# Kernel tuning notes

Hardware: AMD Instinct MI355X
Metric: run time of the kernel (lower is better)

## Reference

```python
import jax, jax.numpy as jnp
import numpy as np

DIM = 256

def setup_inputs() -> dict:
    key = jax.random.key(0)
    ks = jax.random.split(key, 7)
    s = 1.0 / np.sqrt(DIM)
    x = jax.random.normal(ks[0], (16, DIM, 32, 32), dtype=jnp.float32)
    proj_w = jax.random.uniform(ks[1], (DIM, DIM), jnp.float32, -s, s)
    proj_b = jax.random.uniform(ks[2], (DIM,), jnp.float32, -s, s)
    w1 = jax.random.uniform(ks[3], (DIM, DIM), jnp.float32, -s, s)
    b1 = jax.random.uniform(ks[4], (DIM,), jnp.float32, -s, s)
    w2 = jax.random.uniform(ks[5], (DIM, DIM), jnp.float32, -s, s)
    b2 = jax.random.uniform(ks[6], (DIM,), jnp.float32, -s, s)
    return {"x": x, "proj_w": proj_w, "proj_b": proj_b, "w1": w1, "b1": b1, "w2": w2, "b2": b2}

def reference(x, proj_w, proj_b, w1, b1, w2, b2):
    B, C, H, W = x.shape
    # nodes: [B, N, C] with N = H*W
    nodes = x.reshape(B, C, H * W).transpose(0, 2, 1)
    q = nodes @ proj_w.T + proj_b                      # [B,N,C]
    scores = jnp.einsum('bnc,bmc->bnm', q, q) / jnp.sqrt(jnp.float32(C))
    attn = jax.nn.softmax(scores, axis=-1)             # [B,N,N]
    agg = jnp.einsum('bnm,bmc->bnc', attn, nodes)      # [B,N,C]
    h = jax.nn.gelu(agg @ w1.T + b1, approximate=False)
    out = h @ w2.T + b2                                # [B,N,C]
    return x + out.transpose(0, 2, 1).reshape(B, C, H, W)
```

## Files before the change

kernel.cpp:

```cpp
#include <hip/hip_runtime.h>
#include <stdint.h>

typedef unsigned short u16;
typedef unsigned char u8;
typedef __attribute__((ext_vector_type(8))) short short8;
typedef __attribute__((ext_vector_type(4))) float f32x4;

#define NB    16
#define DIM   256
#define NTOK  1024

__device__ __forceinline__ u16 f2b(float f) {
    union { float f; uint32_t u; } v; v.f = f;
    uint32_t u = v.u;
    u += 0x7fffu + ((u >> 16) & 1u);
    return (u16)(u >> 16);
}
__device__ __forceinline__ uint32_t pack2(float a, float b) {
    return (uint32_t)f2b(a) | ((uint32_t)f2b(b) << 16);
}
__device__ __forceinline__ f32x4 mfma16(short8 a, short8 b, f32x4 c) {
    return __builtin_amdgcn_mfma_f32_16x16x32_bf16(a, b, c, 0, 0, 0);
}
__device__ __forceinline__ f32x4 mfma_fp8(long a, long b, f32x4 c) {
    return __builtin_amdgcn_mfma_f32_16x16x32_fp8_fp8(a, b, c, 0, 0, 0);
}
__device__ __forceinline__ short8 ld8(const u16* p) {
    return *reinterpret_cast<const short8*>(p);
}
__device__ __forceinline__ uint32_t pk4fp8(float a, float b, float c, float d) {
    uint32_t u = (uint32_t)__builtin_amdgcn_cvt_pk_fp8_f32(a, b, 0, false);
    u = (uint32_t)__builtin_amdgcn_cvt_pk_fp8_f32(c, d, (int)u, true);
    return u;
}
__device__ __forceinline__ u8 pk1fp8(float a) {
    return (u8)(__builtin_amdgcn_cvt_pk_fp8_f32(a, a, 0, false) & 0xff);
}
__device__ __forceinline__ void gl_lds(const void* g, void* l) {
    __builtin_amdgcn_global_load_lds((const __attribute__((address_space(1))) void*)g,
                                     (__attribute__((address_space(3))) void*)l, 16, 0, 0);
}

__global__ __launch_bounds__(256) void wconv_kernel(const float* __restrict__ pw,
                                                    const float* __restrict__ w1,
                                                    const float* __restrict__ w2,
                                                    u16* __restrict__ wbf) {
    int e = blockIdx.x * 2048 + threadIdx.x * 8;
    const float* s; int off;
    if (e < 65536)       { s = pw; off = e; }
    else if (e < 131072) { s = w1; off = e - 65536; }
    else                 { s = w2; off = e - 131072; }
    float4 f0 = *reinterpret_cast<const float4*>(s + off);
    float4 f1 = *reinterpret_cast<const float4*>(s + off + 4);
    ushort4 a, b;
    a.x = f2b(f0.x); a.y = f2b(f0.y); a.z = f2b(f0.z); a.w = f2b(f0.w);
    b.x = f2b(f1.x); b.y = f2b(f1.y); b.z = f2b(f1.z); b.w = f2b(f1.w);
    *reinterpret_cast<ushort4*>(wbf + e)     = a;
    *reinterpret_cast<ushort4*>(wbf + e + 4) = b;
}

__global__ __launch_bounds__(256) void packproj_kernel(const float* __restrict__ x,
                                                       u8* __restrict__ xbf8,
                                                       const u16* __restrict__ wbf,
                                                       const float* __restrict__ pb,
                                                       u8* __restrict__ qb8) {
    __shared__ float stage[64][68];
    __shared__ u16 tile[64 * 256];
    int tid = threadIdx.x;
    int lane = tid & 63;
    int w = tid >> 6;
    int lo = lane & 15, hi = lane >> 4;
    int b  = blockIdx.x & 15;
    int nt = blockIdx.x >> 4;
    int n0 = nt * 64;
    const float* xb = x + (size_t)b * (DIM * NTOK);
    u8* xbb8 = xbf8 + (size_t)b * (DIM * NTOK);

#pragma unroll
    for (int cc = 0; cc < 4; cc++) {
#pragma unroll
        for (int i = 0; i < 4; i++) {
            int idx = i * 256 + tid;
            int cl = idx >> 4, nq = idx & 15;
            float4 f = *reinterpret_cast<const float4*>(
                xb + (size_t)(cc * 64 + cl) * NTOK + n0 + nq * 4);
            stage[cl][nq * 4 + 0] = f.x;
            stage[cl][nq * 4 + 1] = f.y;
            stage[cl][nq * 4 + 2] = f.z;
            stage[cl][nq * 4 + 3] = f.w;
            *reinterpret_cast<uint32_t*>(xbb8 + (size_t)(cc * 64 + cl) * NTOK + n0 + nq * 4) =
                pk4fp8(f.x, f.y, f.z, f.w);
        }
        __syncthreads();
#pragma unroll
        for (int j = 0; j < 2; j++) {
            int item = j * 256 + tid;
            int nl = item >> 3, g = item & 7;
            union { u16 s[8]; short8 v; } o;
#pragma unroll
            for (int k = 0; k < 8; k++) o.s[k] = f2b(stage[g * 8 + k][nl]);
            int gi = (cc * 8 + g) ^ (nl & 7);
            *reinterpret_cast<short8*>(&tile[nl * 256 + gi * 8]) = o.v;
        }
        __syncthreads();
    }

    f32x4 acc[16];
#pragma unroll
    for (int i = 0; i < 16; i++) acc[i] = (f32x4){0.f, 0.f, 0.f, 0.f};
    int ar = w * 16 + lo;
#pragma unroll
    for (int t = 0; t < 8; t++) {
        int gi = (t * 4 + hi) ^ (lo & 7);
        short8 a = ld8(&tile[ar * 256 + gi * 8]);
#pragma unroll
        for (int nf = 0; nf < 16; nf++) {
            short8 bfr = ld8(wbf + (nf * 16 + lo) * DIM + t * 32 + hi * 8);
            acc[nf] = mfma16(a, bfr, acc[nf]);
        }
    }
#pragma unroll
    for (int nf = 0; nf < 16; nf++) {
        int col = nf * 16 + lo;
        float bias = pb[col];
#pragma unroll
        for (int r = 0; r < 4; r++) {
            int row = n0 + w * 16 + hi * 4 + r;
            qb8[(size_t)(b * NTOK + row) * DIM + col] = pk1fp8(acc[nf][r] + bias);
        }
    }
}

__global__ __launch_bounds__(256, 2) void attn_ffn_kernel(const u8* __restrict__ qb8,
                                                          const u8* __restrict__ xbf8,
                                                          const u16* __restrict__ wbf,
                                                          const float* __restrict__ b1,
                                                          const float* __restrict__ b2,
                                                          const float* __restrict__ x,
                                                          float* __restrict__ out) {
    __shared__ u8 kvls[65536];
    __shared__ float ellX[4][16];

    int lane = threadIdx.x & 63;
    int w = threadIdx.x >> 6;
    int qsel = w >> 1, kvh = w & 1;
    int lo = lane & 15, hi = lane >> 4;
    int b  = blockIdx.x & 15;
    int qt = blockIdx.x >> 4;
    int q0 = qt * 32 + qsel * 16;
    const u8* qbb = qb8  + (size_t)b * (NTOK * DIM);
    const u8* xbb = xbf8 + (size_t)b * (DIM * NTOK);
    const u16* w1b = wbf + 65536;
    const u16* w2b = wbf + 131072;

    int kOff[4], vOff[4], kDst[4], vDst[4];
#pragma unroll
    for (int i = 0; i < 4; i++) {
        int kr = qsel * 16 + i * 4 + (lane >> 4);
        kOff[i] = kr * 256 + ((lane & 15) ^ (kr & 15)) * 16;
        kDst[i] = (qsel * 16 + i * 4) * 256;
        int vc = qsel * 128 + i * 32 + (lane >> 1);
        vOff[i] = vc * 1024 + ((lane & 1) ^ (vc & 1)) * 16;
        vDst[i] = (qsel * 128 + i * 32) * 32;
    }
    int kvbeg = kvh * 512;
    u8* kls0 = &kvls[(kvh * 2) * 8192];
    u8* kls1 = &kvls[(kvh * 2 + 1) * 8192];
    u8* vls0 = &kvls[32768 + (kvh * 2) * 8192];
    u8* vls1 = &kvls[32768 + (kvh * 2 + 1) * 8192];

    long bq[8];
#pragma unroll
    for (int t = 0; t < 8; t++)
        bq[t] = *reinterpret_cast<const long*>(qbb + (size_t)(q0 + lo) * 256 + t * 32 + hi * 8);

    f32x4 acc[16];
#pragma unroll
    for (int i = 0; i < 16; i++) acc[i] = (f32x4){0.f, 0.f, 0.f, 0.f};
    float ellp = 0.f;
    const float C1 = 0.0625f * 1.44269504f;
    const float OFF = 4.0f;

#pragma unroll
    for (int i = 0; i < 4; i++) {
        gl_lds(qbb + kvbeg * 256 + kOff[i], kls0 + kDst[i]);
        gl_lds(xbb + kvbeg       + vOff[i], vls0 + vDst[i]);
    }
    __syncthreads();

    for (int tt = 0; tt < 16; tt++) {
        int buf = tt & 1;
        const u8* kb = buf ? kls1 : kls0;
        const u8* vb = buf ? vls1 : vls0;
        if (tt < 15) {
            int base = kvbeg + (tt + 1) * 32;
            u8* kn = buf ? kls0 : kls1;
            u8* vn = buf ? vls0 : vls1;
#pragma unroll
            for (int i = 0; i < 4; i++) {
                gl_lds(qbb + base * 256 + kOff[i], kn + kDst[i]);
                gl_lds(xbb + base       + vOff[i], vn + vDst[i]);
            }
        }

        f32x4 s0 = (f32x4){0.f,0.f,0.f,0.f};
        f32x4 s1 = (f32x4){0.f,0.f,0.f,0.f};
        __builtin_amdgcn_s_setprio(1);
#pragma unroll
        for (int t = 0; t < 8; t++) {
            int gsw = ((t * 2 + (hi >> 1)) ^ lo) * 16 + (hi & 1) * 8;
            long a0 = *reinterpret_cast<const long*>(kb + lo * 256 + gsw);
            long a1 = *reinterpret_cast<const long*>(kb + (16 + lo) * 256 + gsw);
            s0 = mfma_fp8(a0, bq[t], s0);
            s1 = mfma_fp8(a1, bq[t], s1);
        }
        __builtin_amdgcn_s_setprio(0);

        float p0[4], p1[4];
#pragma unroll
        for (int r = 0; r < 4; r++) {
            p0[r] = exp2f(s0[r] * C1 - OFF);
            p1[r] = exp2f(s1[r] * C1 - OFF);
            ellp += p0[r] + p1[r];
        }

        int srcA = ((2 * hi) & 3) * 16 + lo;
        int srcB = srcA + 16;
        uint32_t d0 = pk4fp8(p0[0], p0[1], p0[2], p0[3]);
        uint32_t d1 = pk4fp8(p1[0], p1[1], p1[2], p1[3]);
        uint32_t a0s = __shfl(d0, srcA), a1s = __shfl(d1, srcA);
        uint32_t a0t = __shfl(d0, srcB), a1t = __shfl(d1, srcB);
        union { uint32_t u[2]; long l; } pu;
        pu.u[0] = (hi < 2) ? a0s : a1s;
        pu.u[1] = (hi < 2) ? a0t : a1t;
        long pf = pu.l;

        int voff = (((hi >> 1) ^ (lo & 1)) * 16) + (hi & 1) * 8;
        __builtin_amdgcn_s_setprio(1);
#pragma unroll
        for (int mf = 0; mf < 16; mf++) {
            long vf = *reinterpret_cast<const long*>(vb + (mf * 16 + lo) * 32 + voff);
            acc[mf] = mfma_fp8(vf, pf, acc[mf]);
        }
        __builtin_amdgcn_s_setprio(0);
        __syncthreads();
    }

    float e = ellp;
    e += __shfl_xor(e, 16);
    e += __shfl_xor(e, 32);
    if (lane < 16) ellX[w][lane] = e;

    char* pbase = (char*)kvls;
    if (kvh == 0) {
#pragma unroll
        for (int j = 0; j < 8; j++) {
            int byt = w * 8192 + lo * 512 + ((j * 64 + hi * 16) ^ ((lo & 7) << 4));
            *reinterpret_cast<f32x4*>(pbase + byt) = acc[8 + j];
        }
    } else {
#pragma unroll
        for (int j = 0; j < 8; j++) {
            int byt = w * 8192 + lo * 512 + ((j * 64 + hi * 16) ^ ((lo & 7) << 4));
            *reinterpret_cast<f32x4*>(pbase + byt) = acc[j];
        }
    }
    __syncthreads();
    float rinv = 1.f / (e + ellX[w ^ 1][lo]);
    char* abase = (char*)kvls + 32768;
    int arow = qsel * 16 + lo;
    if (kvh == 0) {
#pragma unroll
        for (int j = 0; j < 8; j++) {
            int byt = (w ^ 1) * 8192 + lo * 512 + ((j * 64 + hi * 16) ^ ((lo & 7) << 4));
            f32x4 o = *reinterpret_cast<const f32x4*>(pbase + byt);
            uint32_t lo32 = pack2((acc[j][0] + o[0]) * rinv, (acc[j][1] + o[1]) * rinv);
            uint32_t hi32 = pack2((acc[j][2] + o[2]) * rinv, (acc[j][3] + o[3]) * rinv);
            int slot = j * 2 + (hi >> 1);
            int byteA = arow * 512 + ((slot ^ (lo & 7)) * 16) + (hi & 1) * 8;
            *reinterpret_cast<uint32_t*>(abase + byteA)     = lo32;
            *reinterpret_cast<uint32_t*>(abase + byteA + 4) = hi32;
        }
    } else {
#pragma unroll
        for (int j = 0; j < 8; j++) {
            int byt = (w ^ 1) * 8192 + lo * 512 + ((j * 64 + hi * 16) ^ ((lo & 7) << 4));
            f32x4 o = *reinterpret_cast<const f32x4*>(pbase + byt);
            uint32_t lo32 = pack2((acc[8 + j][0] + o[0]) * rinv, (acc[8 + j][1] + o[1]) * rinv);
            uint32_t hi32 = pack2((acc[8 + j][2] + o[2]) * rinv, (acc[8 + j][3] + o[3]) * rinv);
            int slot = 16 + j * 2 + (hi >> 1);
            int byteA = arow * 512 + ((slot ^ (lo & 7)) * 16) + (hi & 1) * 8;
            *reinterpret_cast<uint32_t*>(abase + byteA)     = lo32;
            *reinterpret_cast<uint32_t*>(abase + byteA + 4) = hi32;
        }
    }
    __syncthreads();

    int rh = w & 1, chh = w >> 1;
    f32x4 f1[8];
#pragma unroll
    for (int i = 0; i < 8; i++) f1[i] = (f32x4){0.f, 0.f, 0.f, 0.f};
#pragma unroll
    for (int t = 0; t < 8; t++) {
        int g = ((t * 4 + hi) ^ (lo & 7)) * 16;
        short8 a = *reinterpret_cast<const short8*>(abase + (rh * 16 + lo) * 512 + g);
#pragma unroll
        for (int nf = 0; nf < 8; nf++) {
            short8 bfr = ld8(w1b + ((chh * 8 + nf) * 16 + lo) * DIM + t * 32 + hi * 8);
            f1[nf] = mfma16(a, bfr, f1[nf]);
        }
    }
    u16* hl = (u16*)kvls;
#pragma unroll
    for (int nf = 0; nf < 8; nf++) {
        int f = (chh * 8 + nf) * 16 + lo;
        float bias = b1[f];
#pragma unroll
        for (int r = 0; r < 4; r++) {
            float v = f1[nf][r] + bias;
            float g = 0.5f * v * (1.f + erff(v * 0.70710678f));
            hl[(rh * 16 + hi * 4 + r) * 264 + f] = f2b(g);
        }
    }
    __syncthreads();

    f32x4 f2[8];
#pragma unroll
    for (int i = 0; i < 8; i++) f2[i] = (f32x4){0.f, 0.f, 0.f, 0.f};
#pragma unroll
    for (int t = 0; t < 8; t++) {
        short8 bh = ld8(hl + (rh * 16 + lo) * 264 + t * 32 + hi * 8);
#pragma unroll
        for (int mf = 0; mf < 8; mf++) {
            short8 a2 = ld8(w2b + ((chh * 8 + mf) * 16 + lo) * DIM + t * 32 + hi * 8);
            f2[mf] = mfma16(a2, bh, f2[mf]);
        }
    }
    int n = qt * 32 + rh * 16 + lo;
#pragma unroll
    for (int mf = 0; mf < 8; mf++) {
#pragma unroll
        for (int r = 0; r < 4; r++) {
            int co = (chh * 8 + mf) * 16 + hi * 4 + r;
            size_t addr = (size_t)b * (DIM * NTOK) + (size_t)co * NTOK + n;
            out[addr] = f2[mf][r] + b2[co] + x[addr];
        }
    }
}

extern "C" void kernel_launch(void* const* d_in, const int* in_sizes, int n_in,
                              void* d_out, int out_size, void* d_ws, size_t ws_size,
                              hipStream_t stream) {
    const float* x      = (const float*)d_in[0];
    const float* proj_w = (const float*)d_in[1];
    const float* proj_b = (const float*)d_in[2];
    const float* w1     = (const float*)d_in[3];
    const float* b1     = (const float*)d_in[4];
    const float* w2     = (const float*)d_in[5];
    const float* b2     = (const float*)d_in[6];
    float* out = (float*)d_out;

    u8*  xbf8 = (u8*)d_ws;
    u8*  qb8  = xbf8 + 4194304;
    u16* wbf  = (u16*)(qb8 + 4194304);

    wconv_kernel   <<<96,  256, 0, stream>>>(proj_w, w1, w2, wbf);
    packproj_kernel<<<256, 256, 0, stream>>>(x, xbf8, wbf, proj_b, qb8);
    attn_ffn_kernel<<<512, 256, 0, stream>>>(qb8, xbf8, wbf, b1, b2, x, out);
}
```

Measured before the change: 96.92 us.

## Give each wave all keys for 16 queries, 64-query blocks, 256 workgroups

Restructures the attention kernel so that each of the 4 waves handles 16 distinct queries over the full key range, instead of pairs of waves splitting keys and merging partial accumulators through LDS. Each block now covers 64 queries with 64-key tiles, and the grid is halved to 256 blocks. The FFN stage reuses each weight fragment across two 16-row tiles. This removes the cross-wave reduction and its syncs and doubles weight reuse, but it halves the number of blocks (256 on a 256-CU part) and raises LDS use to about 130KB with launch bounds of 1 block per CU, cutting occupancy and latency hiding.

Result: no change. 97.92 us (+1.0%).

```diff
diff --git a/kernel.cpp b/kernel.cpp
--- a/kernel.cpp
+++ b/kernel.cpp
@@ -131,23 +131,24 @@
     }
 }
 
-__global__ __launch_bounds__(256, 2) void attn_ffn_kernel(const u8* __restrict__ qb8,
+__global__ __launch_bounds__(256, 1) void attn_ffn_kernel(const u8* __restrict__ qb8,
                                                           const u8* __restrict__ xbf8,
                                                           const u16* __restrict__ wbf,
                                                           const float* __restrict__ b1,
                                                           const float* __restrict__ b2,
                                                           const float* __restrict__ x,
                                                           float* __restrict__ out) {
-    __shared__ u8 kvls[65536];
-    __shared__ float ellX[4][16];
+    __shared__ u8  kls[2][16384];
+    __shared__ u8  vls[2][16384];
+    __shared__ u8  aggts[32768];
+    __shared__ u16 hl[64 * 264];
 
     int lane = threadIdx.x & 63;
     int w = threadIdx.x >> 6;
-    int qsel = w >> 1, kvh = w & 1;
     int lo = lane & 15, hi = lane >> 4;
     int b  = blockIdx.x & 15;
     int qt = blockIdx.x >> 4;
-    int q0 = qt * 32 + qsel * 16;
+    int q0 = qt * 64 + w * 16;
     const u8* qbb = qb8  + (size_t)b * (NTOK * DIM);
     const u8* xbb = xbf8 + (size_t)b * (DIM * NTOK);
     const u16* w1b = wbf + 65536;
@@ -156,18 +157,13 @@
     int kOff[4], vOff[4], kDst[4], vDst[4];
 #pragma unroll
     for (int i = 0; i < 4; i++) {
-        int kr = qsel * 16 + i * 4 + (lane >> 4);
+        int kr = w * 16 + i * 4 + (lane >> 4);
         kOff[i] = kr * 256 + ((lane & 15) ^ (kr & 15)) * 16;
-        kDst[i] = (qsel * 16 + i * 4) * 256;
-        int vc = qsel * 128 + i * 32 + (lane >> 1);
-        vOff[i] = vc * 1024 + ((lane & 1) ^ (vc & 1)) * 16;
-        vDst[i] = (qsel * 128 + i * 32) * 32;
-    }
-    int kvbeg = kvh * 512;
-    u8* kls0 = &kvls[(kvh * 2) * 8192];
-    u8* kls1 = &kvls[(kvh * 2 + 1) * 8192];
-    u8* vls0 = &kvls[32768 + (kvh * 2) * 8192];
-    u8* vls1 = &kvls[32768 + (kvh * 2 + 1) * 8192];
+        kDst[i] = (w * 16 + i * 4) * 256;
+        int vc = w * 64 + i * 16 + (lane >> 2);
+        vOff[i] = vc * 1024 + ((lane & 3) ^ (vc & 3)) * 16;
+        vDst[i] = (w * 64 + i * 16) * 64;
+    }
 
     long bq[8];
 #pragma unroll
@@ -183,64 +179,87 @@
 
 #pragma unroll
     for (int i = 0; i < 4; i++) {
-        gl_lds(qbb + kvbeg * 256 + kOff[i], kls0 + kDst[i]);
-        gl_lds(xbb + kvbeg       + vOff[i], vls0 + vDst[i]);
+        gl_lds(qbb + kOff[i], &kls[0][kDst[i]]);
+        gl_lds(xbb + vOff[i], &vls[0][vDst[i]]);
     }
     __syncthreads();
 
     for (int tt = 0; tt < 16; tt++) {
         int buf = tt & 1;
-        const u8* kb = buf ? kls1 : kls0;
-        const u8* vb = buf ? vls1 : vls0;
         if (tt < 15) {
-            int base = kvbeg + (tt + 1) * 32;
-            u8* kn = buf ? kls0 : kls1;
-            u8* vn = buf ? vls0 : vls1;
+            int base = (tt + 1) * 64;
 #pragma unroll
             for (int i = 0; i < 4; i++) {
-                gl_lds(qbb + base * 256 + kOff[i], kn + kDst[i]);
-                gl_lds(xbb + base       + vOff[i], vn + vDst[i]);
+                gl_lds(qbb + base * 256 + kOff[i], &kls[buf ^ 1][kDst[i]]);
+                gl_lds(xbb + base       + vOff[i], &vls[buf ^ 1][vDst[i]]);
             }
         }
+        const u8* kb = &kls[buf][0];
+        const u8* vb = &vls[buf][0];
 
         f32x4 s0 = (f32x4){0.f,0.f,0.f,0.f};
         f32x4 s1 = (f32x4){0.f,0.f,0.f,0.f};
+        f32x4 s2 = (f32x4){0.f,0.f,0.f,0.f};
+        f32x4 s3 = (f32x4){0.f,0.f,0.f,0.f};
         __builtin_amdgcn_s_setprio(1);
 #pragma unroll
         for (int t = 0; t < 8; t++) {
             int gsw = ((t * 2 + (hi >> 1)) ^ lo) * 16 + (hi & 1) * 8;
             long a0 = *reinterpret_cast<const long*>(kb + lo * 256 + gsw);
             long a1 = *reinterpret_cast<const long*>(kb + (16 + lo) * 256 + gsw);
+            long a2 = *reinterpret_cast<const long*>(kb + (32 + lo) * 256 + gsw);
+            long a3 = *reinterpret_cast<const long*>(kb + (48 + lo) * 256 + gsw);
             s0 = mfma_fp8(a0, bq[t], s0);
             s1 = mfma_fp8(a1, bq[t], s1);
+            s2 = mfma_fp8(a2, bq[t], s2);
+            s3 = mfma_fp8(a3, bq[t], s3);
         }
         __builtin_amdgcn_s_setprio(0);
 
-        float p0[4], p1[4];
+        float p0[4], p1[4], p2[4], p3[4];
 #pragma unroll
         for (int r = 0; r < 4; r++) {
             p0[r] = exp2f(s0[r] * C1 - OFF);
             p1[r] = exp2f(s1[r] * C1 - OFF);
-            ellp += p0[r] + p1[r];
+            p2[r] = exp2f(s2[r] * C1 - OFF);
+            p3[r] = exp2f(s3[r] * C1 - OFF);
+            ellp += (p0[r] + p1[r]) + (p2[r] + p3[r]);
         }
 
         int srcA = ((2 * hi) & 3) * 16 + lo;
         int srcB = srcA + 16;
-        uint32_t d0 = pk4fp8(p0[0], p0[1], p0[2], p0[3]);
-        uint32_t d1 = pk4fp8(p1[0], p1[1], p1[2], p1[3]);
-        uint32_t a0s = __shfl(d0, srcA), a1s = __shfl(d1, srcA);
-        uint32_t a0t = __shfl(d0, srcB), a1t = __shfl(d1, srcB);
-        union { uint32_t u[2]; long l; } pu;
-        pu.u[0] = (hi < 2) ? a0s : a1s;
-        pu.u[1] = (hi < 2) ? a0t : a1t;
-        long pf = pu.l;
-
-        int voff = (((hi >> 1) ^ (lo & 1)) * 16) + (hi & 1) * 8;
+        long pfA, pfB;
+        {
+            uint32_t d0 = pk4fp8(p0[0], p0[1], p0[2], p0[3]);
+            uint32_t d1 = pk4fp8(p1[0], p1[1], p1[2], p1[3]);
+            uint32_t a0s = __shfl(d0, srcA), a1s = __shfl(d1, srcA);
+            uint32_t a0t = __shfl(d0, srcB), a1t = __shfl(d1, srcB);
+            union { uint32_t u[2]; long l; } pu;
+            pu.u[0] = (hi < 2) ? a0s : a1s;
+            pu.u[1] = (hi < 2) ? a0t : a1t;
+            pfA = pu.l;
+        }
+        {
+            uint32_t d0 = pk4fp8(p2[0], p2[1], p2[2], p2[3]);
+            uint32_t d1 = pk4fp8(p3[0], p3[1], p3[2], p3[3]);
+            uint32_t a0s = __shfl(d0, srcA), a1s = __shfl(d1, srcA);
+            uint32_t a0t = __shfl(d0, srcB), a1t = __shfl(d1, srcB);
+            union { uint32_t u[2]; long l; } pu;
+            pu.u[0] = (hi < 2) ? a0s : a1s;
+            pu.u[1] = (hi < 2) ? a0t : a1t;
+            pfB = pu.l;
+        }
+
+        int voffA = (((hi >> 1)    ) ^ (lo & 3)) * 16 + (hi & 1) * 8;
+        int voffB = (((hi >> 1) + 2) ^ (lo & 3)) * 16 + (hi & 1) * 8;
         __builtin_amdgcn_s_setprio(1);
 #pragma unroll
         for (int mf = 0; mf < 16; mf++) {
-            long vf = *reinterpret_cast<const long*>(vb + (mf * 16 + lo) * 32 + voff);
-            acc[mf] = mfma_fp8(vf, pf, acc[mf]);
+            const u8* vrow = vb + (mf * 16 + lo) * 64;
+            long vfA = *reinterpret_cast<const long*>(vrow + voffA);
+            long vfB = *reinterpret_cast<const long*>(vrow + voffB);
+            acc[mf] = mfma_fp8(vfA, pfA, acc[mf]);
+            acc[mf] = mfma_fp8(vfB, pfB, acc[mf]);
         }
         __builtin_amdgcn_s_setprio(0);
         __syncthreads();
@@ -249,101 +268,83 @@
     float e = ellp;
     e += __shfl_xor(e, 16);
     e += __shfl_xor(e, 32);
-    if (lane < 16) ellX[w][lane] = e;
-
-    char* pbase = (char*)kvls;
-    if (kvh == 0) {
-#pragma unroll
-        for (int j = 0; j < 8; j++) {
-            int byt = w * 8192 + lo * 512 + ((j * 64 + hi * 16) ^ ((lo & 7) << 4));
-            *reinterpret_cast<f32x4*>(pbase + byt) = acc[8 + j];
-        }
-    } else {
-#pragma unroll
-        for (int j = 0; j < 8; j++) {
-            int byt = w * 8192 + lo * 512 + ((j * 64 + hi * 16) ^ ((lo & 7) << 4));
-            *reinterpret_cast<f32x4*>(pbase + byt) = acc[j];
-        }
+    float rinv = 1.f / e;
+
+    char* abase = (char*)aggts;
+    int arow = w * 16 + lo;
+#pragma unroll
+    for (int j = 0; j < 16; j++) {
+        uint32_t lo32 = pack2(acc[j][0] * rinv, acc[j][1] * rinv);
+        uint32_t hi32 = pack2(acc[j][2] * rinv, acc[j][3] * rinv);
+        int slot = j * 2 + (hi >> 1);
+        int byteA = arow * 512 + ((slot ^ (lo & 7)) * 16) + (hi & 1) * 8;
+        *reinterpret_cast<uint32_t*>(abase + byteA)     = lo32;
+        *reinterpret_cast<uint32_t*>(abase + byteA + 4) = hi32;
     }
     __syncthreads();
-    float rinv = 1.f / (e + ellX[w ^ 1][lo]);
-    char* abase = (char*)kvls + 32768;
-    int arow = qsel * 16 + lo;
-    if (kvh == 0) {
-#pragma unroll
-        for (int j = 0; j < 8; j++) {
-            int byt = (w ^ 1) * 8192 + lo * 512 + ((j * 64 + hi * 16) ^ ((lo & 7) << 4));
-            f32x4 o = *reinterpret_cast<const f32x4*>(pbase + byt);
-            uint32_t lo32 = pack2((acc[j][0] + o[0]) * rinv, (acc[j][1] + o[1]) * rinv);
-            uint32_t hi32 = pack2((acc[j][2] + o[2]) * rinv, (acc[j][3] + o[3]) * rinv);
-            int slot = j * 2 + (hi >> 1);
-            int byteA = arow * 512 + ((slot ^ (lo & 7)) * 16) + (hi & 1) * 8;
-            *reinterpret_cast<uint32_t*>(abase + byteA)     = lo32;
-            *reinterpret_cast<uint32_t*>(abase + byteA + 4) = hi32;
-        }
-    } else {
-#pragma unroll
-        for (int j = 0; j < 8; j++) {
-            int byt = (w ^ 1) * 8192 + lo * 512 + ((j * 64 + hi * 16) ^ ((lo & 7) << 4));
-            f32x4 o = *reinterpret_cast<const f32x4*>(pbase + byt);
-            uint32_t lo32 = pack2((acc[8 + j][0] + o[0]) * rinv, (acc[8 + j][1] + o[1]) * rinv);
-            uint32_t hi32 = pack2((acc[8 + j][2] + o[2]) * rinv, (acc[8 + j][3] + o[3]) * rinv);
-            int slot = 16 + j * 2 + (hi >> 1);
-            int byteA = arow * 512 + ((slot ^ (lo & 7)) * 16) + (hi & 1) * 8;
-            *reinterpret_cast<uint32_t*>(abase + byteA)     = lo32;
-            *reinterpret_cast<uint32_t*>(abase + byteA + 4) = hi32;
-        }
-    }
-    __syncthreads();
-
-    int rh = w & 1, chh = w >> 1;
-    f32x4 f1[8];
-#pragma unroll
-    for (int i = 0; i < 8; i++) f1[i] = (f32x4){0.f, 0.f, 0.f, 0.f};
+
+    int rh = w >> 1, chh = w & 1;
+    f32x4 f1a[8], f1b[8];
+#pragma unroll
+    for (int i = 0; i < 8; i++) {
+        f1a[i] = (f32x4){0.f, 0.f, 0.f, 0.f};
+        f1b[i] = (f32x4){0.f, 0.f, 0.f, 0.f};
+    }
 #pragma unroll
     for (int t = 0; t < 8; t++) {
         int g = ((t * 4 + hi) ^ (lo & 7)) * 16;
-        short8 a = *reinterpret_cast<const short8*>(abase + (rh * 16 + lo) * 512 + g);
+        short8 aA = *reinterpret_cast<const short8*>(abase + (rh * 32 + lo) * 512 + g);
+        short8 aB = *reinterpret_cast<const short8*>(abase + (rh * 32 + 16 + lo) * 512 + g);
 #pragma unroll
         for (int nf = 0; nf < 8; nf++) {
             short8 bfr = ld8(w1b + ((chh * 8 + nf) * 16 + lo) * DIM + t * 32 + hi * 8);
-            f1[nf] = mfma16(a, bfr, f1[nf]);
-        }
-    }
-    u16* hl = (u16*)kvls;
+            f1a[nf] = mfma16(aA, bfr, f1a[nf]);
+            f1b[nf] = mfma16(aB, bfr, f1b[nf]);
+        }
+    }
 #pragma unroll
     for (int nf = 0; nf < 8; nf++) {
         int f = (chh * 8 + nf) * 16 + lo;
         float bias = b1[f];
 #pragma unroll
         for (int r = 0; r < 4; r++) {
-            float v = f1[nf][r] + bias;
-            float g = 0.5f * v * (1.f + erff(v * 0.70710678f));
-            hl[(rh * 16 + hi * 4 + r) * 264 + f] = f2b(g);
+            float va = f1a[nf][r] + bias;
+            float vb2 = f1b[nf][r] + bias;
+            float ga = 0.5f * va * (1.f + erff(va * 0.70710678f));
+            float gb = 0.5f * vb2 * (1.f + erff(vb2 * 0.70710678f));
+            hl[(rh * 32 + hi * 4 + r) * 264 + f]      = f2b(ga);
+            hl[(rh * 32 + 16 + hi * 4 + r) * 264 + f] = f2b(gb);
         }
     }
     __syncthreads();
 
-    f32x4 f2[8];
-#pragma unroll
-    for (int i = 0; i < 8; i++) f2[i] = (f32x4){0.f, 0.f, 0.f, 0.f};
+    f32x4 f2a[8], f2b_[8];
+#pragma unroll
+    for (int i = 0; i < 8; i++) {
+        f2a[i] = (f32x4){0.f, 0.f, 0.f, 0.f};
+        f2b_[i] = (f32x4){0.f, 0.f, 0.f, 0.f};
+    }
 #pragma unroll
     for (int t = 0; t < 8; t++) {
-        short8 bh = ld8(hl + (rh * 16 + lo) * 264 + t * 32 + hi * 8);
+        short8 hA = ld8(hl + (rh * 32 + lo) * 264 + t * 32 + hi * 8);
+        short8 hB = ld8(hl + (rh * 32 + 16 + lo) * 264 + t * 32 + hi * 8);
 #pragma unroll
         for (int mf = 0; mf < 8; mf++) {
             short8 a2 = ld8(w2b + ((chh * 8 + mf) * 16 + lo) * DIM + t * 32 + hi * 8);
-            f2[mf] = mfma16(a2, bh, f2[mf]);
-        }
-    }
-    int n = qt * 32 + rh * 16 + lo;
+            f2a[mf] = mfma16(a2, hA, f2a[mf]);
+            f2b_[mf] = mfma16(a2, hB, f2b_[mf]);
+        }
+    }
+    int nA = qt * 64 + rh * 32 + lo;
+    int nB = nA + 16;
 #pragma unroll
     for (int mf = 0; mf < 8; mf++) {
 #pragma unroll
         for (int r = 0; r < 4; r++) {
             int co = (chh * 8 + mf) * 16 + hi * 4 + r;
-            size_t addr = (size_t)b * (DIM * NTOK) + (size_t)co * NTOK + n;
-            out[addr] = f2[mf][r] + b2[co] + x[addr];
+            size_t rowb = (size_t)b * (DIM * NTOK) + (size_t)co * NTOK;
+            out[rowb + nA] = f2a[mf][r] + b2[co] + x[rowb + nA];
+            out[rowb + nB] = f2b_[mf][r] + b2[co] + x[rowb + nB];
         }
     }
 }
@@ -366,5 +367,5 @@
 
     wconv_kernel   <<<96,  256, 0, stream>>>(proj_w, w1, w2, wbf);
     packproj_kernel<<<256, 256, 0, stream>>>(x, xbf8, wbf, proj_b, qb8);
-    attn_ffn_kernel<<<512, 256, 0, stream>>>(qb8, xbf8, wbf, b1, b2, x, out);
-}
+    attn_ffn_kernel<<<256, 256, 0, stream>>>(qb8, xbf8, wbf, b1, b2, x, out);
+}
```
